# Optimization experiments

Measured on AMD Instinct MI355X. Metric: run time of the kernel, lower is better.

The kernel has to match this reference:

```python
import jax, jax.numpy as jnp
import numpy as np

N, E, F, H = 50000, 1_600_000, 6, 64


def setup_inputs() -> dict:
    key = jax.random.key(0)
    ks = jax.random.split(key, 12)
    inp = {
        "vertex_features": jax.random.normal(ks[0], (N, F), dtype=jnp.float32),
        "edges": jax.random.randint(ks[1], (2, E), 0, N, dtype=jnp.int64 if jax.config.jax_enable_x64 else jnp.int32),
        "weights": jax.random.uniform(ks[2], (E,), dtype=jnp.float32),
        # GCNConv layer params (glorot-ish scale) + biases (PyG default bias=True)
        "W1": jax.random.normal(ks[3], (F, H), dtype=jnp.float32) / np.sqrt(F),
        "b1": jnp.zeros((H,), jnp.float32),
        "W2": jax.random.normal(ks[4], (H, H), dtype=jnp.float32) / np.sqrt(H),
        "b2": jnp.zeros((H,), jnp.float32),
        "W3": jax.random.normal(ks[5], (H, H), dtype=jnp.float32) / np.sqrt(H),
        "b3": jnp.zeros((H,), jnp.float32),
        "Wl": jax.random.normal(ks[6], (H, 1), dtype=jnp.float32) / np.sqrt(H),
        "bl": jnp.zeros((1,), jnp.float32),
    }
    return inp


def _gcn_norm(edges, weights, n):
    # PyG gcn_norm: add self loops (weight 1), symmetric D^-1/2 A D^-1/2;
    # degree computed at target nodes (edge_index[1], flow source_to_target).
    row, col = edges[0], edges[1]
    loop = jnp.arange(n, dtype=row.dtype)
    row_f = jnp.concatenate([row, loop])
    col_f = jnp.concatenate([col, loop])
    w_f = jnp.concatenate([weights, jnp.ones((n,), weights.dtype)])
    deg = jax.ops.segment_sum(w_f, col_f, num_segments=n)
    dis = jnp.where(deg > 0, jax.lax.rsqrt(jnp.maximum(deg, 1e-30)), 0.0)
    norm = dis[row_f] * w_f * dis[col_f]
    return row_f, col_f, norm


def _gcn_conv(x, W, b, row, col, norm, n):
    xw = x @ W                                   # [n, H_out]
    agg = jax.ops.segment_sum(norm[:, None] * xw[row], col, num_segments=n)
    return agg + b


def reference(vertex_features, edges, weights, W1, b1, W2, b2, W3, b3, Wl, bl):
    n = vertex_features.shape[0]
    row, col, norm = _gcn_norm(edges, weights, n)  # norm identical for all layers
    h = jax.nn.sigmoid(_gcn_conv(vertex_features, W1, b1, row, col, norm, n))
    h = jax.nn.sigmoid(_gcn_conv(h, W2, b2, row, col, norm, n))
    h = jax.nn.sigmoid(_gcn_conv(h, W3, b3, row, col, norm, n))
    logits = h @ Wl + bl                           # [n, 1]
    return jax.nn.softmax(logits, axis=0)          # softmax over node dim
```

## Files before the change

kernel.cpp:

```cpp
#include <hip/hip_runtime.h>
#include <math.h>


#define BLK 256
#define SKB 256
#define CHUNK 4096

typedef __attribute__((ext_vector_type(8))) short bf16x8;
typedef __attribute__((ext_vector_type(4))) float f32x4;

__device__ inline unsigned short f2bf(float f) {
  unsigned u = __float_as_uint(f);
  return (unsigned short)((u + 0x7FFF + ((u >> 16) & 1)) >> 16);
}
__device__ inline float bflo(unsigned u) { return __uint_as_float(u << 16); }
__device__ inline float bfhi(unsigned u) { return __uint_as_float(u & 0xFFFF0000u); }


__global__ __launch_bounds__(256) void k_binscatter(
    const int* __restrict__ row, const int* __restrict__ col,
    const float* __restrict__ w, int E,
    int* __restrict__ bfill, int2* __restrict__ bucket, int CAP) {
  __shared__ int2 stage[CHUNK];
  __shared__ int lhist[SKB], lbase[SKB], gbase[SKB], lfill[SKB];
  int t = threadIdx.x;
  int e0 = blockIdx.x * CHUNK;
  int n = E - e0; if (n > CHUNK) n = CHUNK;
  lhist[t] = 0; lfill[t] = 0;
  __syncthreads();
  for (int i = t; i < n; i += BLK) atomicAdd(&lhist[((unsigned)col[e0 + i]) >> 8], 1);
  __syncthreads();
  lbase[t] = lhist[t];
  __syncthreads();
  for (int off = 1; off < SKB; off <<= 1) {
    int v = (t >= off) ? lbase[t - off] : 0;
    __syncthreads();
    lbase[t] += v;
    __syncthreads();
  }
  int excl = lbase[t] - lhist[t];
  int cb = lhist[t];
  gbase[t] = cb ? atomicAdd(&bfill[t << 4], cb) : 0;
  __syncthreads();
  lbase[t] = excl;
  __syncthreads();
  for (int i = t; i < n; i += BLK) {
    int c = col[e0 + i];
    int b = ((unsigned)c) >> 8;
    int r = atomicAdd(&lfill[b], 1);
    stage[lbase[b] + r] = make_int2(row[e0 + i] | (c << 16), __float_as_int(w[e0 + i]));
  }
  __syncthreads();
  for (int i = t; i < n; i += BLK) {
    int2 p = stage[i];
    int b = ((unsigned)p.x) >> 24;
    bucket[(size_t)b * CAP + gbase[b] + (i - lbase[b])] = p;
  }
}


__global__ __launch_bounds__(256) void k_build(
    const int2* __restrict__ bucket, const int* __restrict__ bfill,
    const float* __restrict__ x,
    unsigned* __restrict__ csr, int* __restrict__ cnt, int* __restrict__ start,
    float* __restrict__ dis, unsigned short* __restrict__ x8b, int CAP, int N) {
  __shared__ int   hist[SKB];
  __shared__ float wsum[SKB];
  __shared__ int   lstart[SKB + 1];
  __shared__ int   lfill[SKB];
  int b = blockIdx.x, t = threadIdx.x;
  int n0 = b << 8;
  int M = N - n0; if (M > 256) M = 256;
  if (M <= 0) return;
  hist[t] = 0; wsum[t] = 0.0f; lfill[t] = 0;
  __syncthreads();
  const int2* bb = bucket + (size_t)b * CAP;
  int ec = bfill[b << 4];
  for (int i = t; i < ec; i += BLK) {
    int2 p = bb[i];
    int lc = (((unsigned)p.x) >> 16) & 255;
    atomicAdd(&hist[lc], 1);
    atomicAdd(&wsum[lc], __int_as_float(p.y));
  }
  __syncthreads();
  if (t == 0) {
    int run = 0;
    for (int i = 0; i < M; ++i) { lstart[i] = run; run += hist[i]; }
    lstart[M] = run;
  }
  __syncthreads();
  if (t < M) {
    int n = n0 + t;
    cnt[n] = hist[t];
    start[n] = b * CAP + lstart[t];
    float d = 1.0f / sqrtf(wsum[t] + 1.0f);
    dis[n] = d;
    const float* xr = x + (size_t)n * 6;
    uint4 pk;
    pk.x = (unsigned)f2bf(d * xr[0]) | ((unsigned)f2bf(d * xr[1]) << 16);
    pk.y = (unsigned)f2bf(d * xr[2]) | ((unsigned)f2bf(d * xr[3]) << 16);
    pk.z = (unsigned)f2bf(d * xr[4]) | ((unsigned)f2bf(d * xr[5]) << 16);
    pk.w = 0u;
    *(uint4*)(x8b + (size_t)n * 8) = pk;
  }
  __syncthreads();
  for (int i = t; i < ec; i += BLK) {
    int2 p = bb[i];
    int lc = (((unsigned)p.x) >> 16) & 255;
    int pos = lstart[lc] + atomicAdd(&lfill[lc], 1);
    csr[(size_t)b * CAP + pos] =
        ((unsigned)p.x & 0xFFFFu) | ((unsigned)f2bf(__int_as_float(p.y)) << 16);
  }
}


__global__ void k_wprep(const float* __restrict__ W2, const float* __restrict__ W3,
                        unsigned short* __restrict__ W2b, unsigned short* __restrict__ W3b) {
  int i = blockIdx.x * blockDim.x + threadIdx.x;
  if (i < 4096) { W2b[i] = f2bf(W2[i]); W3b[i] = f2bf(W3[i]); }
}


__global__ void k_layer1(const unsigned short* __restrict__ x8b,
                         const int* __restrict__ start, const int* __restrict__ cnt,
                         const unsigned* __restrict__ csr, const float* __restrict__ dis,
                         const float* __restrict__ W1, const float* __restrict__ b1,
                         unsigned short* __restrict__ hb, int N) {
  int n = blockIdx.x * blockDim.x + threadIdx.x;
  if (n >= N) return;
  uint4 sv = *(const uint4*)(x8b + (size_t)n * 8);
  float a0 = bflo(sv.x), a1 = bfhi(sv.x), a2 = bflo(sv.y);
  float a3 = bfhi(sv.y), a4 = bflo(sv.z), a5 = bfhi(sv.z);
  int s = start[n], e = s + cnt[n];
  int i = s;
  for (; i + 4 <= e; i += 4) {
    unsigned p0 = csr[i], p1 = csr[i + 1], p2 = csr[i + 2], p3 = csr[i + 3];
    uint4 h0 = *(const uint4*)(x8b + (size_t)(p0 & 0xFFFFu) * 8);
    uint4 h1 = *(const uint4*)(x8b + (size_t)(p1 & 0xFFFFu) * 8);
    uint4 h2 = *(const uint4*)(x8b + (size_t)(p2 & 0xFFFFu) * 8);
    uint4 h3 = *(const uint4*)(x8b + (size_t)(p3 & 0xFFFFu) * 8);
    float v0 = bfhi(p0), v1 = bfhi(p1), v2 = bfhi(p2), v3 = bfhi(p3);
    a0 += v0*bflo(h0.x) + v1*bflo(h1.x) + v2*bflo(h2.x) + v3*bflo(h3.x);
    a1 += v0*bfhi(h0.x) + v1*bfhi(h1.x) + v2*bfhi(h2.x) + v3*bfhi(h3.x);
    a2 += v0*bflo(h0.y) + v1*bflo(h1.y) + v2*bflo(h2.y) + v3*bflo(h3.y);
    a3 += v0*bfhi(h0.y) + v1*bfhi(h1.y) + v2*bfhi(h2.y) + v3*bfhi(h3.y);
    a4 += v0*bflo(h0.z) + v1*bflo(h1.z) + v2*bflo(h2.z) + v3*bflo(h3.z);
    a5 += v0*bfhi(h0.z) + v1*bfhi(h1.z) + v2*bfhi(h2.z) + v3*bfhi(h3.z);
  }
  for (; i < e; ++i) {
    unsigned pe = csr[i];
    float v = bfhi(pe);
    uint4 hv = *(const uint4*)(x8b + (size_t)(pe & 0xFFFFu) * 8);
    a0 += v * bflo(hv.x); a1 += v * bfhi(hv.x);
    a2 += v * bflo(hv.y); a3 += v * bfhi(hv.y);
    a4 += v * bflo(hv.z); a5 += v * bfhi(hv.z);
  }
  float d = dis[n];
  a0 *= d; a1 *= d; a2 *= d; a3 *= d; a4 *= d; a5 *= d;
  unsigned short* o = hb + (size_t)n * 64;
#pragma unroll
  for (int j4 = 0; j4 < 16; ++j4) {
    float4 acc = *(const float4*)(b1 + j4 * 4);
    const float* Wc = W1 + j4 * 4;
    acc.x += a0*Wc[0] + a1*Wc[64] + a2*Wc[128] + a3*Wc[192] + a4*Wc[256] + a5*Wc[320];
    acc.y += a0*Wc[1] + a1*Wc[65] + a2*Wc[129] + a3*Wc[193] + a4*Wc[257] + a5*Wc[321];
    acc.z += a0*Wc[2] + a1*Wc[66] + a2*Wc[130] + a3*Wc[194] + a4*Wc[258] + a5*Wc[322];
    acc.w += a0*Wc[3] + a1*Wc[67] + a2*Wc[131] + a3*Wc[195] + a4*Wc[259] + a5*Wc[323];
    uint2 pk;
    pk.x = (unsigned)f2bf(d / (1.0f + expf(-acc.x))) |
           ((unsigned)f2bf(d / (1.0f + expf(-acc.y))) << 16);
    pk.y = (unsigned)f2bf(d / (1.0f + expf(-acc.z))) |
           ((unsigned)f2bf(d / (1.0f + expf(-acc.w))) << 16);
    *(uint2*)(o + j4 * 4) = pk;
  }
}


__global__ void k_agg64(const unsigned short* __restrict__ hb,
                        const int* __restrict__ start, const int* __restrict__ cnt,
                        const unsigned* __restrict__ csr, const float* __restrict__ dis,
                        unsigned short* __restrict__ aggb, int N) {
  int t = blockIdx.x * blockDim.x + threadIdx.x;
  int n = t >> 3, sub = t & 7;
  if (n >= N) return;
  uint4 sv = *(const uint4*)(hb + (size_t)n * 64 + sub * 8);
  float a0 = bflo(sv.x), a1 = bfhi(sv.x), a2 = bflo(sv.y), a3 = bfhi(sv.y);
  float a4 = bflo(sv.z), a5 = bfhi(sv.z), a6 = bflo(sv.w), a7 = bfhi(sv.w);
  int s = start[n], e = s + cnt[n];
  int i = s;
  for (; i + 4 <= e; i += 4) {
    unsigned p0 = csr[i], p1 = csr[i + 1], p2 = csr[i + 2], p3 = csr[i + 3];
    uint4 h0 = *(const uint4*)(hb + (size_t)(p0 & 0xFFFFu) * 64 + sub * 8);
    uint4 h1 = *(const uint4*)(hb + (size_t)(p1 & 0xFFFFu) * 64 + sub * 8);
    uint4 h2 = *(const uint4*)(hb + (size_t)(p2 & 0xFFFFu) * 64 + sub * 8);
    uint4 h3 = *(const uint4*)(hb + (size_t)(p3 & 0xFFFFu) * 64 + sub * 8);
    float v0 = bfhi(p0), v1 = bfhi(p1), v2 = bfhi(p2), v3 = bfhi(p3);
    a0 += v0*bflo(h0.x) + v1*bflo(h1.x) + v2*bflo(h2.x) + v3*bflo(h3.x);
    a1 += v0*bfhi(h0.x) + v1*bfhi(h1.x) + v2*bfhi(h2.x) + v3*bfhi(h3.x);
    a2 += v0*bflo(h0.y) + v1*bflo(h1.y) + v2*bflo(h2.y) + v3*bflo(h3.y);
    a3 += v0*bfhi(h0.y) + v1*bfhi(h1.y) + v2*bfhi(h2.y) + v3*bfhi(h3.y);
    a4 += v0*bflo(h0.z) + v1*bflo(h1.z) + v2*bflo(h2.z) + v3*bflo(h3.z);
    a5 += v0*bfhi(h0.z) + v1*bfhi(h1.z) + v2*bfhi(h2.z) + v3*bfhi(h3.z);
    a6 += v0*bflo(h0.w) + v1*bflo(h1.w) + v2*bflo(h2.w) + v3*bflo(h3.w);
    a7 += v0*bfhi(h0.w) + v1*bfhi(h1.w) + v2*bfhi(h2.w) + v3*bfhi(h3.w);
  }
  for (; i < e; ++i) {
    unsigned pe = csr[i];
    float v = bfhi(pe);
    uint4 hv = *(const uint4*)(hb + (size_t)(pe & 0xFFFFu) * 64 + sub * 8);
    a0 += v * bflo(hv.x); a1 += v * bfhi(hv.x);
    a2 += v * bflo(hv.y); a3 += v * bfhi(hv.y);
    a4 += v * bflo(hv.z); a5 += v * bfhi(hv.z);
    a6 += v * bflo(hv.w); a7 += v * bfhi(hv.w);
  }
  float d = dis[n];
  uint4 pk;
  pk.x = (unsigned)f2bf(d * a0) | ((unsigned)f2bf(d * a1) << 16);
  pk.y = (unsigned)f2bf(d * a2) | ((unsigned)f2bf(d * a3) << 16);
  pk.z = (unsigned)f2bf(d * a4) | ((unsigned)f2bf(d * a5) << 16);
  pk.w = (unsigned)f2bf(d * a6) | ((unsigned)f2bf(d * a7) << 16);
  *(uint4*)(aggb + (size_t)n * 64 + sub * 8) = pk;
}


__global__ __launch_bounds__(256) void k_dense64_mfma(
    const unsigned short* __restrict__ aggb, const unsigned short* __restrict__ Wb,
    const float* __restrict__ b, const float* __restrict__ dis,
    unsigned short* __restrict__ hb, int NS) {
  int wid = threadIdx.x >> 6, lane = threadIdx.x & 63;
  int quad = lane >> 4, r16 = lane & 15;
  bf16x8 Bf[2][4];
#pragma unroll
  for (int kt = 0; kt < 2; ++kt)
#pragma unroll
    for (int jt = 0; jt < 4; ++jt)
#pragma unroll
      for (int j = 0; j < 8; ++j)
        Bf[kt][jt][j] = (short)Wb[(kt * 32 + quad * 8 + j) * 64 + jt * 16 + r16];
  float bias[4];
#pragma unroll
  for (int jt = 0; jt < 4; ++jt) bias[jt] = b[jt * 16 + r16];
  int stride = gridDim.x * 4;
  for (int s = blockIdx.x * 4 + wid; s < NS; s += stride) {
    int n0 = s * 16;
    bf16x8 Af0 = *(const bf16x8*)(aggb + (size_t)(n0 + r16) * 64 + quad * 8);
    bf16x8 Af1 = *(const bf16x8*)(aggb + (size_t)(n0 + r16) * 64 + 32 + quad * 8);
    f32x4 C[4];
#pragma unroll
    for (int jt = 0; jt < 4; ++jt) {
      f32x4 z = {0.f, 0.f, 0.f, 0.f};
      z = __builtin_amdgcn_mfma_f32_16x16x32_bf16(Af0, Bf[0][jt], z, 0, 0, 0);
      z = __builtin_amdgcn_mfma_f32_16x16x32_bf16(Af1, Bf[1][jt], z, 0, 0, 0);
      C[jt] = z;
    }
    float dv[4];
#pragma unroll
    for (int reg = 0; reg < 4; ++reg) dv[reg] = dis[n0 + quad * 4 + reg];
#pragma unroll
    for (int jt = 0; jt < 4; ++jt)
#pragma unroll
      for (int reg = 0; reg < 4; ++reg) {
        float h = dv[reg] / (1.0f + expf(-(C[jt][reg] + bias[jt])));
        hb[(size_t)(n0 + quad * 4 + reg) * 64 + jt * 16 + r16] = f2bf(h);
      }
  }
}


__global__ __launch_bounds__(256) void k_head_mfma(
    const unsigned short* __restrict__ aggb, const unsigned short* __restrict__ Wb,
    const float* __restrict__ b, const float* __restrict__ Wl,
    const float* __restrict__ bl, float* __restrict__ expv,
    float* __restrict__ red_part, int NS) {
  int wid = threadIdx.x >> 6, lane = threadIdx.x & 63;
  int quad = lane >> 4, r16 = lane & 15;
  bf16x8 Bf[2][4];
#pragma unroll
  for (int kt = 0; kt < 2; ++kt)
#pragma unroll
    for (int jt = 0; jt < 4; ++jt)
#pragma unroll
      for (int j = 0; j < 8; ++j)
        Bf[kt][jt][j] = (short)Wb[(kt * 32 + quad * 8 + j) * 64 + jt * 16 + r16];
  float bias[4], wlv[4];
#pragma unroll
  for (int jt = 0; jt < 4; ++jt) {
    bias[jt] = b[jt * 16 + r16];
    wlv[jt]  = Wl[jt * 16 + r16];
  }
  float bl0 = bl[0];
  float lsum = 0.0f;
  int stride = gridDim.x * 4;
  for (int s = blockIdx.x * 4 + wid; s < NS; s += stride) {
    int n0 = s * 16;
    bf16x8 Af0 = *(const bf16x8*)(aggb + (size_t)(n0 + r16) * 64 + quad * 8);
    bf16x8 Af1 = *(const bf16x8*)(aggb + (size_t)(n0 + r16) * 64 + 32 + quad * 8);
    f32x4 C[4];
#pragma unroll
    for (int jt = 0; jt < 4; ++jt) {
      f32x4 z = {0.f, 0.f, 0.f, 0.f};
      z = __builtin_amdgcn_mfma_f32_16x16x32_bf16(Af0, Bf[0][jt], z, 0, 0, 0);
      z = __builtin_amdgcn_mfma_f32_16x16x32_bf16(Af1, Bf[1][jt], z, 0, 0, 0);
      C[jt] = z;
    }
    float p0 = 0, p1 = 0, p2 = 0, p3 = 0;
#pragma unroll
    for (int jt = 0; jt < 4; ++jt) {
      p0 += wlv[jt] / (1.0f + expf(-(C[jt][0] + bias[jt])));
      p1 += wlv[jt] / (1.0f + expf(-(C[jt][1] + bias[jt])));
      p2 += wlv[jt] / (1.0f + expf(-(C[jt][2] + bias[jt])));
      p3 += wlv[jt] / (1.0f + expf(-(C[jt][3] + bias[jt])));
    }
#pragma unroll
    for (int m = 1; m < 16; m <<= 1) {
      p0 += __shfl_xor(p0, m, 64);
      p1 += __shfl_xor(p1, m, 64);
      p2 += __shfl_xor(p2, m, 64);
      p3 += __shfl_xor(p3, m, 64);
    }
    float ls = 0.0f;
    if (r16 == 0) {
      float e0 = expf(p0 + bl0), e1 = expf(p1 + bl0);
      float e2 = expf(p2 + bl0), e3 = expf(p3 + bl0);
      int r = n0 + quad * 4;
      expv[r] = e0; expv[r + 1] = e1; expv[r + 2] = e2; expv[r + 3] = e3;
      ls = e0 + e1 + e2 + e3;
    }
    ls += __shfl_xor(ls, 16, 64);
    ls += __shfl_xor(ls, 32, 64);
    lsum += ls;
  }
  if (lane == 0) atomicAdd(&red_part[(blockIdx.x & 63) << 4], lsum);
}

__global__ void k_out(const float* __restrict__ expv, int N,
                      const float* __restrict__ red_part, float* __restrict__ out) {
  int i = blockIdx.x * blockDim.x + threadIdx.x;
  int lane = threadIdx.x & 63;
  float s = red_part[lane << 4];
#pragma unroll
  for (int o = 32; o > 0; o >>= 1) s += __shfl_down(s, o, 64);
  s = __shfl(s, 0, 64);
  if (i < N) out[i] = expv[i] / s;
}


extern "C" void kernel_launch(void* const* d_in, const int* in_sizes, int n_in,
                              void* d_out, int out_size, void* d_ws, size_t ws_size,
                              hipStream_t stream) {
  const float* x   = (const float*)d_in[0];
  const int*   edg = (const int*)d_in[1];
  const float* w   = (const float*)d_in[2];
  const float* W1  = (const float*)d_in[3];
  const float* b1  = (const float*)d_in[4];
  const float* W2  = (const float*)d_in[5];
  const float* b2  = (const float*)d_in[6];
  const float* W3  = (const float*)d_in[7];
  const float* b3  = (const float*)d_in[8];
  const float* Wl  = (const float*)d_in[9];
  const float* bl  = (const float*)d_in[10];
  float* out = (float*)d_out;

  const int N = in_sizes[0] / 6;
  const int E = in_sizes[2];
  const int* row = edg;
  const int* col = edg + E;
  const int NB = (N + 255) >> 8;
  const int NS = (N + 15) / 16;

  size_t off = 0;
  char* base = (char*)d_ws;
  auto alloc = [&](size_t bytes) -> void* {
    void* p = base + off;
    off += (bytes + 255) & ~(size_t)255;
    return p;
  };
  int*   bfill    = (int*)alloc((size_t)SKB * 16 * 4);
  float* red_part = (float*)alloc((size_t)64 * 16 * 4);
  size_t zero_bytes = off;
  int*   cnt    = (int*)alloc((size_t)N * 4);
  int*   start  = (int*)alloc((size_t)N * 4);
  float* dis    = (float*)alloc((size_t)N * 4);
  float* expv   = (float*)alloc((size_t)N * 4);
  unsigned short* x8b = (unsigned short*)alloc((size_t)N * 8 * 2);
  unsigned short* hb  = (unsigned short*)alloc((size_t)N * 64 * 2);
  unsigned short* W2b = (unsigned short*)alloc(4096 * 2);
  unsigned short* W3b = (unsigned short*)alloc(4096 * 2);
  size_t remain = (ws_size > off) ? (ws_size - off) : 0;
  long long capn = ((long long)remain) / ((long long)NB * 12);
  int CAP = (int)capn;
  if (CAP > 9216) CAP = 9216;
  if (CAP < 8704) CAP = 8704;
  unsigned* csr = (unsigned*)alloc((size_t)NB * CAP * 4);
  size_t aggsz = (size_t)N * 64 * 2;
  size_t bksz  = (size_t)NB * CAP * 8;
  void* shared_blk = alloc(aggsz > bksz ? aggsz : bksz);
  int2*           bucket = (int2*)shared_blk;
  unsigned short* aggb   = (unsigned short*)shared_blk;

  const int gE  = (E + CHUNK - 1) / CHUNK;
  const int gN  = (N + BLK - 1) / BLK;
  const int gN8 = (N * 8 + BLK - 1) / BLK;
  const int gM  = 200;

  hipMemsetAsync(d_ws, 0, zero_bytes, stream);

  k_wprep     <<<16, BLK, 0, stream>>>(W2, W3, W2b, W3b);
  k_binscatter<<<gE, BLK, 0, stream>>>(row, col, w, E, bfill, bucket, CAP);
  k_build     <<<NB, BLK, 0, stream>>>(bucket, bfill, x, csr, cnt, start, dis, x8b, CAP, N);

  k_layer1<<<gN, BLK, 0, stream>>>(x8b, start, cnt, csr, dis, W1, b1, hb, N);

  k_agg64       <<<gN8, BLK, 0, stream>>>(hb, start, cnt, csr, dis, aggb, N);
  k_dense64_mfma<<<gM,  BLK, 0, stream>>>(aggb, W2b, b2, dis, hb, NS);

  k_agg64    <<<gN8, BLK, 0, stream>>>(hb, start, cnt, csr, dis, aggb, N);
  k_head_mfma<<<gM,  BLK, 0, stream>>>(aggb, W3b, b3, Wl, bl, expv, red_part, NS);

  k_out<<<gN, BLK, 0, stream>>>(expv, N, red_part, out);
}
```

Measured before the change: 232.4 us.

## Split per-node gather across more threads in layer1 and agg64 kernels

Layer 1 now assigns eight threads per node. Each thread gathers a strided subset of edges, the partial sums are combined with xor-shuffles, and each thread computes two of the sixteen output column groups. The 64-wide aggregation now uses sixteen threads per node with 8-byte loads instead of eight threads with 16-byte loads, and its edge loop is unrolled by eight. The goal is more memory-level parallelism and better load balance in the latency-bound gathers. The cost is narrower per-lane accesses, more redundant reads of the CSR indices, and shuffle overhead.

```diff
diff --git a/kernel.cpp b/kernel.cpp
--- a/kernel.cpp
+++ b/kernel.cpp
@@ -126,28 +126,30 @@
                          const unsigned* __restrict__ csr, const float* __restrict__ dis,
                          const float* __restrict__ W1, const float* __restrict__ b1,
                          unsigned short* __restrict__ hb, int N) {
-  int n = blockIdx.x * blockDim.x + threadIdx.x;
+  int t = blockIdx.x * blockDim.x + threadIdx.x;
+  int n = t >> 3, sub = t & 7;
   if (n >= N) return;
-  uint4 sv = *(const uint4*)(x8b + (size_t)n * 8);
-  float a0 = bflo(sv.x), a1 = bfhi(sv.x), a2 = bflo(sv.y);
-  float a3 = bfhi(sv.y), a4 = bflo(sv.z), a5 = bfhi(sv.z);
+  float a0 = 0.f, a1 = 0.f, a2 = 0.f, a3 = 0.f, a4 = 0.f, a5 = 0.f;
+  if (sub == 0) {
+    uint4 sv = *(const uint4*)(x8b + (size_t)n * 8);
+    a0 = bflo(sv.x); a1 = bfhi(sv.x); a2 = bflo(sv.y);
+    a3 = bfhi(sv.y); a4 = bflo(sv.z); a5 = bfhi(sv.z);
+  }
   int s = start[n], e = s + cnt[n];
-  int i = s;
-  for (; i + 4 <= e; i += 4) {
-    unsigned p0 = csr[i], p1 = csr[i + 1], p2 = csr[i + 2], p3 = csr[i + 3];
+  int i = s + sub;
+  for (; i + 8 < e; i += 16) {
+    unsigned p0 = csr[i], p1 = csr[i + 8];
     uint4 h0 = *(const uint4*)(x8b + (size_t)(p0 & 0xFFFFu) * 8);
     uint4 h1 = *(const uint4*)(x8b + (size_t)(p1 & 0xFFFFu) * 8);
-    uint4 h2 = *(const uint4*)(x8b + (size_t)(p2 & 0xFFFFu) * 8);
-    uint4 h3 = *(const uint4*)(x8b + (size_t)(p3 & 0xFFFFu) * 8);
-    float v0 = bfhi(p0), v1 = bfhi(p1), v2 = bfhi(p2), v3 = bfhi(p3);
-    a0 += v0*bflo(h0.x) + v1*bflo(h1.x) + v2*bflo(h2.x) + v3*bflo(h3.x);
-    a1 += v0*bfhi(h0.x) + v1*bfhi(h1.x) + v2*bfhi(h2.x) + v3*bfhi(h3.x);
-    a2 += v0*bflo(h0.y) + v1*bflo(h1.y) + v2*bflo(h2.y) + v3*bflo(h3.y);
-    a3 += v0*bfhi(h0.y) + v1*bfhi(h1.y) + v2*bfhi(h2.y) + v3*bfhi(h3.y);
-    a4 += v0*bflo(h0.z) + v1*bflo(h1.z) + v2*bflo(h2.z) + v3*bflo(h3.z);
-    a5 += v0*bfhi(h0.z) + v1*bfhi(h1.z) + v2*bfhi(h2.z) + v3*bfhi(h3.z);
-  }
-  for (; i < e; ++i) {
+    float v0 = bfhi(p0), v1 = bfhi(p1);
+    a0 += v0 * bflo(h0.x) + v1 * bflo(h1.x);
+    a1 += v0 * bfhi(h0.x) + v1 * bfhi(h1.x);
+    a2 += v0 * bflo(h0.y) + v1 * bflo(h1.y);
+    a3 += v0 * bfhi(h0.y) + v1 * bfhi(h1.y);
+    a4 += v0 * bflo(h0.z) + v1 * bflo(h1.z);
+    a5 += v0 * bfhi(h0.z) + v1 * bfhi(h1.z);
+  }
+  for (; i < e; i += 8) {
     unsigned pe = csr[i];
     float v = bfhi(pe);
     uint4 hv = *(const uint4*)(x8b + (size_t)(pe & 0xFFFFu) * 8);
@@ -155,11 +157,18 @@
     a2 += v * bflo(hv.y); a3 += v * bfhi(hv.y);
     a4 += v * bflo(hv.z); a5 += v * bfhi(hv.z);
   }
+#pragma unroll
+  for (int m = 1; m < 8; m <<= 1) {
+    a0 += __shfl_xor(a0, m, 64); a1 += __shfl_xor(a1, m, 64);
+    a2 += __shfl_xor(a2, m, 64); a3 += __shfl_xor(a3, m, 64);
+    a4 += __shfl_xor(a4, m, 64); a5 += __shfl_xor(a5, m, 64);
+  }
   float d = dis[n];
   a0 *= d; a1 *= d; a2 *= d; a3 *= d; a4 *= d; a5 *= d;
   unsigned short* o = hb + (size_t)n * 64;
 #pragma unroll
-  for (int j4 = 0; j4 < 16; ++j4) {
+  for (int jj = 0; jj < 2; ++jj) {
+    int j4 = sub * 2 + jj;
     float4 acc = *(const float4*)(b1 + j4 * 4);
     const float* Wc = W1 + j4 * 4;
     acc.x += a0*Wc[0] + a1*Wc[64] + a2*Wc[128] + a3*Wc[192] + a4*Wc[256] + a5*Wc[320];
@@ -181,45 +190,46 @@
                         const unsigned* __restrict__ csr, const float* __restrict__ dis,
                         unsigned short* __restrict__ aggb, int N) {
   int t = blockIdx.x * blockDim.x + threadIdx.x;
-  int n = t >> 3, sub = t & 7;
+  int n = t >> 4, sub = t & 15;
   if (n >= N) return;
-  uint4 sv = *(const uint4*)(hb + (size_t)n * 64 + sub * 8);
+  uint2 sv = *(const uint2*)(hb + (size_t)n * 64 + sub * 4);
   float a0 = bflo(sv.x), a1 = bfhi(sv.x), a2 = bflo(sv.y), a3 = bfhi(sv.y);
-  float a4 = bflo(sv.z), a5 = bfhi(sv.z), a6 = bflo(sv.w), a7 = bfhi(sv.w);
   int s = start[n], e = s + cnt[n];
   int i = s;
-  for (; i + 4 <= e; i += 4) {
-    unsigned p0 = csr[i], p1 = csr[i + 1], p2 = csr[i + 2], p3 = csr[i + 3];
-    uint4 h0 = *(const uint4*)(hb + (size_t)(p0 & 0xFFFFu) * 64 + sub * 8);
-    uint4 h1 = *(const uint4*)(hb + (size_t)(p1 & 0xFFFFu) * 64 + sub * 8);
-    uint4 h2 = *(const uint4*)(hb + (size_t)(p2 & 0xFFFFu) * 64 + sub * 8);
-    uint4 h3 = *(const uint4*)(hb + (size_t)(p3 & 0xFFFFu) * 64 + sub * 8);
+  for (; i + 8 <= e; i += 8) {
+    unsigned p0 = csr[i],     p1 = csr[i + 1], p2 = csr[i + 2], p3 = csr[i + 3];
+    unsigned p4 = csr[i + 4], p5 = csr[i + 5], p6 = csr[i + 6], p7 = csr[i + 7];
+    uint2 h0 = *(const uint2*)(hb + (size_t)(p0 & 0xFFFFu) * 64 + sub * 4);
+    uint2 h1 = *(const uint2*)(hb + (size_t)(p1 & 0xFFFFu) * 64 + sub * 4);
+    uint2 h2 = *(const uint2*)(hb + (size_t)(p2 & 0xFFFFu) * 64 + sub * 4);
+    uint2 h3 = *(const uint2*)(hb + (size_t)(p3 & 0xFFFFu) * 64 + sub * 4);
+    uint2 h4 = *(const uint2*)(hb + (size_t)(p4 & 0xFFFFu) * 64 + sub * 4);
+    uint2 h5 = *(const uint2*)(hb + (size_t)(p5 & 0xFFFFu) * 64 + sub * 4);
+    uint2 h6 = *(const uint2*)(hb + (size_t)(p6 & 0xFFFFu) * 64 + sub * 4);
+    uint2 h7 = *(const uint2*)(hb + (size_t)(p7 & 0xFFFFu) * 64 + sub * 4);
     float v0 = bfhi(p0), v1 = bfhi(p1), v2 = bfhi(p2), v3 = bfhi(p3);
-    a0 += v0*bflo(h0.x) + v1*bflo(h1.x) + v2*bflo(h2.x) + v3*bflo(h3.x);
-    a1 += v0*bfhi(h0.x) + v1*bfhi(h1.x) + v2*bfhi(h2.x) + v3*bfhi(h3.x);
-    a2 += v0*bflo(h0.y) + v1*bflo(h1.y) + v2*bflo(h2.y) + v3*bflo(h3.y);
-    a3 += v0*bfhi(h0.y) + v1*bfhi(h1.y) + v2*bfhi(h2.y) + v3*bfhi(h3.y);
-    a4 += v0*bflo(h0.z) + v1*bflo(h1.z) + v2*bflo(h2.z) + v3*bflo(h3.z);
-    a5 += v0*bfhi(h0.z) + v1*bfhi(h1.z) + v2*bfhi(h2.z) + v3*bfhi(h3.z);
-    a6 += v0*bflo(h0.w) + v1*bflo(h1.w) + v2*bflo(h2.w) + v3*bflo(h3.w);
-    a7 += v0*bfhi(h0.w) + v1*bfhi(h1.w) + v2*bfhi(h2.w) + v3*bfhi(h3.w);
+    float v4 = bfhi(p4), v5 = bfhi(p5), v6 = bfhi(p6), v7 = bfhi(p7);
+    a0 += v0*bflo(h0.x) + v1*bflo(h1.x) + v2*bflo(h2.x) + v3*bflo(h3.x)
+        + v4*bflo(h4.x) + v5*bflo(h5.x) + v6*bflo(h6.x) + v7*bflo(h7.x);
+    a1 += v0*bfhi(h0.x) + v1*bfhi(h1.x) + v2*bfhi(h2.x) + v3*bfhi(h3.x)
+        + v4*bfhi(h4.x) + v5*bfhi(h5.x) + v6*bfhi(h6.x) + v7*bfhi(h7.x);
+    a2 += v0*bflo(h0.y) + v1*bflo(h1.y) + v2*bflo(h2.y) + v3*bflo(h3.y)
+        + v4*bflo(h4.y) + v5*bflo(h5.y) + v6*bflo(h6.y) + v7*bflo(h7.y);
+    a3 += v0*bfhi(h0.y) + v1*bfhi(h1.y) + v2*bfhi(h2.y) + v3*bfhi(h3.y)
+        + v4*bfhi(h4.y) + v5*bfhi(h5.y) + v6*bfhi(h6.y) + v7*bfhi(h7.y);
   }
   for (; i < e; ++i) {
     unsigned pe = csr[i];
     float v = bfhi(pe);
-    uint4 hv = *(const uint4*)(hb + (size_t)(pe & 0xFFFFu) * 64 + sub * 8);
+    uint2 hv = *(const uint2*)(hb + (size_t)(pe & 0xFFFFu) * 64 + sub * 4);
     a0 += v * bflo(hv.x); a1 += v * bfhi(hv.x);
     a2 += v * bflo(hv.y); a3 += v * bfhi(hv.y);
-    a4 += v * bflo(hv.z); a5 += v * bfhi(hv.z);
-    a6 += v * bflo(hv.w); a7 += v * bfhi(hv.w);
   }
   float d = dis[n];
-  uint4 pk;
+  uint2 pk;
   pk.x = (unsigned)f2bf(d * a0) | ((unsigned)f2bf(d * a1) << 16);
   pk.y = (unsigned)f2bf(d * a2) | ((unsigned)f2bf(d * a3) << 16);
-  pk.z = (unsigned)f2bf(d * a4) | ((unsigned)f2bf(d * a5) << 16);
-  pk.w = (unsigned)f2bf(d * a6) | ((unsigned)f2bf(d * a7) << 16);
-  *(uint4*)(aggb + (size_t)n * 64 + sub * 8) = pk;
+  *(uint2*)(aggb + (size_t)n * 64 + sub * 4) = pk;
 }
 
 
@@ -398,10 +408,11 @@
   int2*           bucket = (int2*)shared_blk;
   unsigned short* aggb   = (unsigned short*)shared_blk;
 
-  const int gE  = (E + CHUNK - 1) / CHUNK;
-  const int gN  = (N + BLK - 1) / BLK;
-  const int gN8 = (N * 8 + BLK - 1) / BLK;
-  const int gM  = 200;
+  const int gE   = (E + CHUNK - 1) / CHUNK;
+  const int gN   = (N + BLK - 1) / BLK;
+  const int gN8  = (N * 8 + BLK - 1) / BLK;
+  const int gN16 = (N * 16 + BLK - 1) / BLK;
+  const int gM   = 200;
 
   hipMemsetAsync(d_ws, 0, zero_bytes, stream);
 
@@ -409,13 +420,13 @@
   k_binscatter<<<gE, BLK, 0, stream>>>(row, col, w, E, bfill, bucket, CAP);
   k_build     <<<NB, BLK, 0, stream>>>(bucket, bfill, x, csr, cnt, start, dis, x8b, CAP, N);
 
-  k_layer1<<<gN, BLK, 0, stream>>>(x8b, start, cnt, csr, dis, W1, b1, hb, N);
-
-  k_agg64       <<<gN8, BLK, 0, stream>>>(hb, start, cnt, csr, dis, aggb, N);
-  k_dense64_mfma<<<gM,  BLK, 0, stream>>>(aggb, W2b, b2, dis, hb, NS);
-
-  k_agg64    <<<gN8, BLK, 0, stream>>>(hb, start, cnt, csr, dis, aggb, N);
-  k_head_mfma<<<gM,  BLK, 0, stream>>>(aggb, W3b, b3, Wl, bl, expv, red_part, NS);
+  k_layer1<<<gN8, BLK, 0, stream>>>(x8b, start, cnt, csr, dis, W1, b1, hb, N);
+
+  k_agg64       <<<gN16, BLK, 0, stream>>>(hb, start, cnt, csr, dis, aggb, N);
+  k_dense64_mfma<<<gM,   BLK, 0, stream>>>(aggb, W2b, b2, dis, hb, NS);
+
+  k_agg64    <<<gN16, BLK, 0, stream>>>(hb, start, cnt, csr, dis, aggb, N);
+  k_head_mfma<<<gM,   BLK, 0, stream>>>(aggb, W3b, b3, Wl, bl, expv, red_part, NS);
 
   k_out<<<gN, BLK, 0, stream>>>(expv, N, red_part, out);
 }
```

Result: no change. 234.7 us (+1.0%).
